# Kernel optimization log

Hardware: AMD Instinct MI355X
Metric: run time of the kernel (lower is better)

The kernel has to match this reference:

```python
import jax, jax.numpy as jnp
import numpy as np

B, N, D, H = 2, 2048, 1024, 16
HD = D // H

def setup_inputs() -> dict:
    key = jax.random.key(0)
    ks = jax.random.split(key, 8)
    s = lambda fan_in: 1.0 / np.sqrt(fan_in)
    return {
        "x": jax.random.normal(ks[0], (B, N, D), jnp.float32),
        "coverage": jax.random.uniform(ks[1], (B, N, 1), jnp.float32),
        "w_qkv": jax.random.normal(ks[2], (D, 3 * D), jnp.float32) * s(D),
        "w_out": jax.random.normal(ks[3], (D, D), jnp.float32) * s(D),
        "b_out": jnp.zeros((D,), jnp.float32),
        "w_ce1": jax.random.normal(ks[4], (1, D // 4), jnp.float32),
        "b_ce1": jnp.zeros((D // 4,), jnp.float32),
        "w_ce2": jax.random.normal(ks[5], (D // 4, H), jnp.float32) * s(D // 4),
        "b_ce2": jnp.zeros((H,), jnp.float32),
        "w_fg1": jax.random.normal(ks[6], (D, D // 4), jnp.float32) * s(D),
        "b_fg1": jnp.zeros((D // 4,), jnp.float32),
        "w_fg2": jax.random.normal(ks[7], (D // 4, 1), jnp.float32) * s(D // 4),
        "b_fg2": jnp.zeros((1,), jnp.float32),
    }

def reference(x, coverage, w_qkv, w_out, b_out, w_ce1, b_ce1, w_ce2, b_ce2,
              w_fg1, b_fg1, w_fg2, b_fg2):
    b, n, d = x.shape
    h = w_ce2.shape[1]
    hd = d // h
    scale = hd ** -0.5
    qkv = x @ w_qkv  # (B,N,3D)
    q, k, v = jnp.split(qkv, 3, axis=-1)
    q = q.reshape(b, n, h, hd).transpose(0, 2, 1, 3)  # (B,H,N,hd)
    k = k.reshape(b, n, h, hd).transpose(0, 2, 1, 3)
    v = v.reshape(b, n, h, hd).transpose(0, 2, 1, 3)
    attn = jnp.einsum("bhnd,bhmd->bhnm", q, k) * scale  # (B,H,N,N)
    # coverage bias: MLP(1 -> D/4 -> H), broadcast over query dim
    cov = jax.nn.silu(coverage @ w_ce1 + b_ce1) @ w_ce2 + b_ce2  # (B,N,H)
    cov_bias = cov.transpose(0, 2, 1)[:, :, None, :]  # (B,H,1,N)
    # fusion gate on mean-pooled features
    x_pooled = x.mean(axis=1)  # (B,D)
    g = jax.nn.sigmoid(jax.nn.silu(x_pooled @ w_fg1 + b_fg1) @ w_fg2 + b_fg2)  # (B,1)
    g = g[:, :, None, None]  # (B,1,1,1)
    # g*(attn+bias) + (1-g)*attn == attn + g*bias (exact same math)
    attn = attn + g * cov_bias
    attn = jax.nn.softmax(attn, axis=-1)
    out = jnp.einsum("bhnm,bhmd->bhnd", attn, v)  # (B,H,N,hd)
    out = out.transpose(0, 2, 1, 3).reshape(b, n, d)
    return out @ w_out + b_out
```

## Files before the change

### kernel.cpp

```cpp
#include <hip/hip_runtime.h>
#include <math.h>

typedef __bf16 bf16_t;
typedef __bf16 bf16x8 __attribute__((ext_vector_type(8)));
typedef __bf16 bf16x4 __attribute__((ext_vector_type(4)));
typedef float f32x4 __attribute__((ext_vector_type(4)));

#define MFMA16(a, b, c) __builtin_amdgcn_mfma_f32_16x16x32_bf16((a), (b), (c), 0, 0, 0)

constexpr int Bc = 2, Nc = 2048, Dc = 1024, Hc = 16, HDc = 64;
constexpr float C1 = 0.18033688011112042f;
constexpr float LOG2E = 1.4426950408889634f;

__device__ __forceinline__ void glds16(const bf16_t* g, bf16_t* l) {
    __builtin_amdgcn_global_load_lds(
        (const __attribute__((address_space(1))) unsigned int*)g,
        (__attribute__((address_space(3))) unsigned int*)l, 16, 0, 0);
}

__device__ __forceinline__ void tr64_body(const float* __restrict__ src,
                                          bf16_t* __restrict__ dst, int R, int C,
                                          int bx, int by, bf16_t* tile, int t) {
    int r0 = by * 64, c0 = bx * 64;
    int cl = t & 63, rl = t >> 6;
#pragma unroll
    for (int p = 0; p < 16; ++p) {
        int r = p * 4 + rl;
        tile[r * 66 + cl] = (bf16_t)src[(size_t)(r0 + r) * C + c0 + cl];
    }
    __syncthreads();
#pragma unroll
    for (int p = 0; p < 16; ++p) {
        int r = p * 4 + rl;
        dst[(size_t)(c0 + r) * R + r0 + cl] = tile[cl * 66 + r];
    }
}

__global__ __launch_bounds__(256) void prep(const float* __restrict__ x,
                                            bf16_t* __restrict__ Xb,
                                            const float* __restrict__ w_qkv,
                                            bf16_t* __restrict__ Wt,
                                            const float* __restrict__ w_out,
                                            bf16_t* __restrict__ WoT,
                                            float* __restrict__ pooled,
                                            const float* __restrict__ coverage,
                                            const float* __restrict__ w_ce1,
                                            const float* __restrict__ b_ce1,
                                            const float* __restrict__ w_ce2,
                                            const float* __restrict__ b_ce2,
                                            float* __restrict__ cbias) {
    __shared__ __align__(16) float smem[8768];
    int bid = blockIdx.x, t = threadIdx.x;

    if (bid < 64) {
        float* w1s = smem;
        float* b1s = smem + 256;
        float* w2s = smem + 512;
        float* part = smem + 4608;
        int b = bid >> 5, n0 = (bid & 31) * 64;
        w1s[t] = w_ce1[t];
        b1s[t] = b_ce1[t];
        {
            float4* w2v = (float4*)w2s;
            const float4* g4 = (const float4*)w_ce2;
#pragma unroll
            for (int i = 0; i < 4; ++i) w2v[i * 256 + t] = g4[i * 256 + t];
        }
        __syncthreads();
        int wv = t >> 6, lane2 = t & 63;
        float c = coverage[b * 2048 + n0 + lane2];
        float acc[16];
#pragma unroll
        for (int hh = 0; hh < 16; ++hh) acc[hh] = 0.f;
        for (int jj = 0; jj < 64; ++jj) {
            int j = wv * 64 + jj;
            float tv = fmaf(c, w1s[j], b1s[j]);
            tv = tv / (1.0f + __expf(-tv));
#pragma unroll
            for (int hh = 0; hh < 16; ++hh)
                acc[hh] = fmaf(tv, w2s[j * 16 + hh], acc[hh]);
        }
#pragma unroll
        for (int hh = 0; hh < 16; ++hh) part[lane2 * 65 + wv * 16 + hh] = acc[hh];
        __syncthreads();
#pragma unroll
        for (int i = 0; i < 4; ++i) {
            int idx = t + i * 256;
            int nl = idx >> 4, hh = idx & 15;
            const float* pr = part + nl * 65 + hh;
            float s = pr[0] + pr[16] + pr[32] + pr[48];
            cbias[((size_t)b * 16 + hh) * 2048 + n0 + nl] = LOG2E * (s + b_ce2[hh]);
        }
    } else if (bid < 320) {
        int blk = bid - 64;
        int b = blk >> 7, ch = blk & 127;
        int c = t * 4;
        float s0 = 0.f, s1 = 0.f, s2 = 0.f, s3 = 0.f;
        for (int rr = 0; rr < 16; ++rr) {
            float4 v = *(const float4*)(x + (size_t)(b * Nc + ch * 16 + rr) * Dc + c);
            s0 += v.x; s1 += v.y; s2 += v.z; s3 += v.w;
        }
        atomicAdd(&pooled[b * Dc + c + 0], s0);
        atomicAdd(&pooled[b * Dc + c + 1], s1);
        atomicAdd(&pooled[b * Dc + c + 2], s2);
        atomicAdd(&pooled[b * Dc + c + 3], s3);
    } else if (bid < 1088) {
        int bb = bid - 320;
        tr64_body(w_qkv, Wt, 1024, 3072, bb % 48, bb / 48, (bf16_t*)smem, t);
    } else if (bid < 1344) {
        int bb = bid - 1088;
        tr64_body(w_out, WoT, 1024, 1024, bb & 15, bb >> 4, (bf16_t*)smem, t);
    } else {
        int base = (bid - 1344) * 4096 + t * 4;
#pragma unroll
        for (int c = 0; c < 4; ++c) {
            int i = base + c * 1024;
            float4 v = *(const float4*)(x + i);
            bf16x4 o = { (bf16_t)v.x, (bf16_t)v.y, (bf16_t)v.z, (bf16_t)v.w };
            *(bf16x4*)(Xb + i) = o;
        }
    }
}

__global__ __launch_bounds__(256) void qkv_gemm(const bf16_t* __restrict__ Xb,
                                                const bf16_t* __restrict__ Wt,
                                                bf16_t* __restrict__ Q,
                                                bf16_t* __restrict__ Kb,
                                                bf16_t* __restrict__ Vt,
                                                const float* __restrict__ pooled,
                                                const float* __restrict__ w_fg1,
                                                const float* __restrict__ b_fg1,
                                                const float* __restrict__ w_fg2,
                                                float* __restrict__ hacc) {
    __shared__ __align__(16) bf16_t At[2][128 * 32];
    __shared__ __align__(16) bf16_t Bt[2][128 * 32];
    int t = threadIdx.x;

    if (blockIdx.y == 24) {
        __shared__ float red[4];
        int blk = blockIdx.x;
        int b = blk >> 4, jb = (blk & 15) * 16;
        for (int jj = 0; jj < 16; ++jj) {
            int j = jb + jj;
            float p = 0.f;
#pragma unroll
            for (int i = 0; i < 4; ++i) {
                int d = t * 4 + i;
                p += pooled[b * 1024 + d] * w_fg1[d * 256 + j];
            }
#pragma unroll
            for (int off = 32; off > 0; off >>= 1) p += __shfl_down(p, off);
            if ((t & 63) == 0) red[t >> 6] = p;
            __syncthreads();
            if (t == 0) {
                float hj = (red[0] + red[1] + red[2] + red[3]) * (1.0f / 2048.0f) + b_fg1[j];
                hj = hj / (1.0f + __expf(-hj));
                atomicAdd(&hacc[b], hj * w_fg2[j]);
            }
            __syncthreads();
        }
        return;
    }

    int w = t >> 6, lane = t & 63;
    int l16 = lane & 15, quad = lane >> 4;
    int wm = w & 1, wx = w >> 1;
    int m0 = blockIdx.x * 128;
    int n0 = blockIdx.y * 128;
    f32x4 acc[4][4] = {};
    int sw = (l16 >> 2) & 3;

    int arow[2], asc[2], aoff[2];
#pragma unroll
    for (int i = 0; i < 2; ++i) {
        int fb = i * 4096 + w * 1024;
        int f = fb + lane * 16;
        int row = f >> 6;
        int ch = (f >> 4) & 3;
        arow[i] = row;
        asc[i] = ch ^ ((row >> 2) & 3);
        aoff[i] = fb >> 1;
    }
    auto stage = [&](int k0, int bf) {
#pragma unroll
        for (int i = 0; i < 2; ++i) {
            glds16(Wt + (size_t)(n0 + arow[i]) * 1024 + k0 + asc[i] * 8, At[bf] + aoff[i]);
            glds16(Xb + (size_t)(m0 + arow[i]) * 1024 + k0 + asc[i] * 8, Bt[bf] + aoff[i]);
        }
    };

    stage(0, 0);
    for (int ks = 0; ks < 32; ++ks) {
        int sel = ks & 1;
        asm volatile("s_waitcnt lgkmcnt(0)" ::: "memory");
        __builtin_amdgcn_s_barrier();
        if (ks + 1 < 32) {
            stage((ks + 1) * 32, sel ^ 1);
            asm volatile("s_waitcnt vmcnt(4)" ::: "memory");
        } else {
            asm volatile("s_waitcnt vmcnt(0)" ::: "memory");
        }
        __builtin_amdgcn_s_barrier();
        __builtin_amdgcn_sched_barrier(0);

        const bf16_t* Ab = At[sel];
        const bf16_t* Bb = Bt[sel];
        bf16x8 afr[4], bfr[4];
#pragma unroll
        for (int mi = 0; mi < 4; ++mi)
            afr[mi] = *(const bf16x8*)(Ab + (wm * 64 + mi * 16 + l16) * 32 + ((quad ^ sw) * 8));
#pragma unroll
        for (int ni = 0; ni < 4; ++ni)
            bfr[ni] = *(const bf16x8*)(Bb + (wx * 64 + ni * 16 + l16) * 32 + ((quad ^ sw) * 8));
        __builtin_amdgcn_s_setprio(1);
#pragma unroll
        for (int mi = 0; mi < 4; ++mi)
#pragma unroll
            for (int ni = 0; ni < 4; ++ni)
                acc[mi][ni] = MFMA16(afr[mi], bfr[ni], acc[mi][ni]);
        __builtin_amdgcn_s_setprio(0);
    }

    int sec = n0 >> 10;
    float scq = (sec == 0) ? C1 : 1.0f;
#pragma unroll
    for (int mi = 0; mi < 4; ++mi) {
        int gc = n0 + wm * 64 + mi * 16 + quad * 4;
        int dcol = gc & 1023;
        int h = dcol >> 6, hd = dcol & 63;
#pragma unroll
        for (int ni = 0; ni < 4; ++ni) {
            int gx = m0 + wx * 64 + ni * 16 + l16;
            int b = gx >> 11, n = gx & 2047;
            size_t bh = (size_t)(b * 16 + h);
            if (sec == 2) {
#pragma unroll
                for (int r = 0; r < 4; ++r)
                    Vt[(bh * 64 + hd + r) * 2048 + n] = (bf16_t)acc[mi][ni][r];
            } else {
                bf16x4 pk = { (bf16_t)(acc[mi][ni][0] * scq), (bf16_t)(acc[mi][ni][1] * scq),
                              (bf16_t)(acc[mi][ni][2] * scq), (bf16_t)(acc[mi][ni][3] * scq) };
                bf16_t* dst = (sec == 0 ? Q : Kb);
                *(bf16x4*)(dst + (bh * 2048 + n) * 64 + hd) = pk;
            }
        }
    }
}

__global__ __launch_bounds__(256) void attn_k(const bf16_t* __restrict__ Q,
                                              const bf16_t* __restrict__ Kb,
                                              const bf16_t* __restrict__ Vt,
                                              const float* __restrict__ cbias,
                                              const float* __restrict__ hacc,
                                              const float* __restrict__ b_fg2,
                                              bf16_t* __restrict__ O) {
    __shared__ __align__(16) bf16_t kbuf[2][64 * 64];
    __shared__ __align__(16) bf16_t vbuf[2][64 * 64];
    __shared__ __align__(16) float ball[2048];
    int t = threadIdx.x, w = t >> 6, lane = t & 63;
    int l16 = lane & 15, quad = lane >> 4;
    int bh = blockIdx.y;
    int b = bh >> 4, h = bh & 15;
    int qa = blockIdx.x * 128 + w * 32;
    const bf16_t* Qh = Q + (size_t)bh * 2048 * 64;
    const bf16_t* Kh = Kb + (size_t)bh * 2048 * 64;
    const bf16_t* Vh = Vt + (size_t)bh * 64 * 2048;
    const float* bih = cbias + (size_t)bh * 2048;
    float g = 1.0f / (1.0f + __expf(-(hacc[b] + b_fg2[0])));

#pragma unroll
    for (int c = 0; c < 2; ++c) {
        float4 v = *(const float4*)(bih + c * 1024 + t * 4);
        float4 sv = { v.x * g, v.y * g, v.z * g, v.w * g };
        *(float4*)(ball + c * 1024 + t * 4) = sv;
    }

    int fb0 = w * 2048, fb1 = fb0 + 1024;
    int f0 = fb0 + lane * 16, f1 = fb1 + lane * 16;
    int krow0 = f0 >> 7, kch0 = ((f0 >> 4) & 7) ^ (krow0 & 7);
    int krow1 = f1 >> 7, kch1 = ((f1 >> 4) & 7) ^ (krow1 & 7);

    bf16x8 qf[2][2];
#pragma unroll
    for (int qt = 0; qt < 2; ++qt)
#pragma unroll
        for (int dh = 0; dh < 2; ++dh)
            qf[qt][dh] = *(const bf16x8*)(Qh + (size_t)(qa + qt * 16 + l16) * 64 + dh * 32 + quad * 8);

    f32x4 o[2][4] = {};
    f32x4 lacc[2] = {};
    bf16x8 onesb;
#pragma unroll
    for (int i = 0; i < 8; ++i) onesb[i] = (bf16_t)1.0f;
    int swl = l16 & 7;
    int qh = quad >> 1, ql = quad & 1;

    int bk0 = l16 * 64 + ((quad ^ swl) * 8);
    int bk1 = l16 * 64 + (((4 + quad) ^ swl) * 8);
    int bv0 = l16 * 64 + ql * 4 + ((qh ^ swl) * 8);
    int bv1 = l16 * 64 + ql * 4 + (((2 + qh) ^ swl) * 8);
    int bv2 = l16 * 64 + ql * 4 + (((4 + qh) ^ swl) * 8);
    int bv3 = l16 * 64 + ql * 4 + (((6 + qh) ^ swl) * 8);

    auto stage = [&](int tile_, int bf) {
        int jn = tile_ * 64;
        glds16(Kh + (size_t)(jn + krow0) * 64 + kch0 * 8, &kbuf[bf][fb0 >> 1]);
        glds16(Kh + (size_t)(jn + krow1) * 64 + kch1 * 8, &kbuf[bf][fb1 >> 1]);
        glds16(Vh + (size_t)krow0 * 2048 + jn + kch0 * 8, &vbuf[bf][fb0 >> 1]);
        glds16(Vh + (size_t)krow1 * 2048 + jn + kch1 * 8, &vbuf[bf][fb1 >> 1]);
    };

    stage(0, 0);

    for (int it = 0; it < 32; ++it) {
        int sel = it & 1, j0 = it * 64;
        asm volatile("s_waitcnt lgkmcnt(0)" ::: "memory");
        __builtin_amdgcn_s_barrier();
        if (it + 1 < 32) {
            stage(it + 1, sel ^ 1);
            asm volatile("s_waitcnt vmcnt(4)" ::: "memory");
        } else {
            asm volatile("s_waitcnt vmcnt(0)" ::: "memory");
        }
        __builtin_amdgcn_s_barrier();
        __builtin_amdgcn_sched_barrier(0);

        const bf16_t* kb = &kbuf[sel][0];
        const bf16_t* vb = &vbuf[sel][0];

        f32x4 s[2][4];
        __builtin_amdgcn_s_setprio(1);
#pragma unroll
        for (int kt = 0; kt < 4; ++kt) {
            f32x4 bi = *(const f32x4*)(ball + j0 + kt * 16 + quad * 4);
            bf16x8 kf0 = *(const bf16x8*)(kb + kt * 1024 + bk0);
            bf16x8 kf1 = *(const bf16x8*)(kb + kt * 1024 + bk1);
#pragma unroll
            for (int qt = 0; qt < 2; ++qt) {
                s[qt][kt] = MFMA16(kf0, qf[qt][0], bi);
                s[qt][kt] = MFMA16(kf1, qf[qt][1], s[qt][kt]);
            }
        }
        __builtin_amdgcn_s_setprio(0);

        bf16x8 pf[2][2];
#pragma unroll
        for (int qt = 0; qt < 2; ++qt) {
#pragma unroll
            for (int kt = 0; kt < 4; ++kt)
#pragma unroll
                for (int r = 0; r < 4; ++r)
                    s[qt][kt][r] = __builtin_amdgcn_exp2f(s[qt][kt][r]);
#pragma unroll
            for (int pv = 0; pv < 2; ++pv) {
                bf16x8 tmp;
#pragma unroll
                for (int i = 0; i < 4; ++i) {
                    tmp[i]     = (bf16_t)s[qt][2 * pv][i];
                    tmp[i + 4] = (bf16_t)s[qt][2 * pv + 1][i];
                }
                pf[qt][pv] = tmp;
            }
        }

        __builtin_amdgcn_s_setprio(1);
#pragma unroll
        for (int qt = 0; qt < 2; ++qt) {
            lacc[qt] = MFMA16(pf[qt][0], onesb, lacc[qt]);
            lacc[qt] = MFMA16(pf[qt][1], onesb, lacc[qt]);
        }
#pragma unroll
        for (int dt = 0; dt < 4; ++dt) {
            bf16x4 va0 = *(const bf16x4*)(vb + dt * 1024 + bv0);
            bf16x4 vc0 = *(const bf16x4*)(vb + dt * 1024 + bv1);
            bf16x8 vf0 = __builtin_shufflevector(va0, vc0, 0, 1, 2, 3, 4, 5, 6, 7);
            bf16x4 va1 = *(const bf16x4*)(vb + dt * 1024 + bv2);
            bf16x4 vc1 = *(const bf16x4*)(vb + dt * 1024 + bv3);
            bf16x8 vf1 = __builtin_shufflevector(va1, vc1, 0, 1, 2, 3, 4, 5, 6, 7);
#pragma unroll
            for (int qt = 0; qt < 2; ++qt) {
                o[qt][dt] = MFMA16(pf[qt][0], vf0, o[qt][dt]);
                o[qt][dt] = MFMA16(pf[qt][1], vf1, o[qt][dt]);
            }
        }
        __builtin_amdgcn_s_setprio(0);
    }

#pragma unroll
    for (int qt = 0; qt < 2; ++qt) {
        f32x4 rinv;
#pragma unroll
        for (int r = 0; r < 4; ++r) rinv[r] = 1.0f / lacc[qt][r];
#pragma unroll
        for (int dt = 0; dt < 4; ++dt)
#pragma unroll
            for (int r = 0; r < 4; ++r) {
                int row = qa + qt * 16 + quad * 4 + r;
                O[(size_t)(b * 2048 + row) * 1024 + h * 64 + dt * 16 + l16] =
                    (bf16_t)(o[qt][dt][r] * rinv[r]);
            }
    }
}

__global__ __launch_bounds__(256) void out_gemm(const bf16_t* __restrict__ A,
                                                const bf16_t* __restrict__ Wt,
                                                const float* __restrict__ bias,
                                                float* __restrict__ Cout) {
    __shared__ __align__(16) bf16_t At[2][128 * 32];
    __shared__ __align__(16) bf16_t Bt[2][128 * 32];
    int t = threadIdx.x, w = t >> 6, lane = t & 63;
    int l16 = lane & 15, quad = lane >> 4;
    int wm = w & 1, wx = w >> 1;
    int m0 = blockIdx.x * 128;
    int n0 = blockIdx.y * 128;
    f32x4 acc[4][4] = {};
    int sw = (l16 >> 2) & 3;

    int arow[2], asc[2], aoff[2];
#pragma unroll
    for (int i = 0; i < 2; ++i) {
        int fb = i * 4096 + w * 1024;
        int f = fb + lane * 16;
        int row = f >> 6;
        int ch = (f >> 4) & 3;
        arow[i] = row;
        asc[i] = ch ^ ((row >> 2) & 3);
        aoff[i] = fb >> 1;
    }
    auto stage = [&](int k0, int bf) {
#pragma unroll
        for (int i = 0; i < 2; ++i) {
            glds16(Wt + (size_t)(n0 + arow[i]) * 1024 + k0 + asc[i] * 8, At[bf] + aoff[i]);
            glds16(A + (size_t)(m0 + arow[i]) * 1024 + k0 + asc[i] * 8, Bt[bf] + aoff[i]);
        }
    };

    stage(0, 0);
    for (int ks = 0; ks < 32; ++ks) {
        int sel = ks & 1;
        asm volatile("s_waitcnt lgkmcnt(0)" ::: "memory");
        __builtin_amdgcn_s_barrier();
        if (ks + 1 < 32) {
            stage((ks + 1) * 32, sel ^ 1);
            asm volatile("s_waitcnt vmcnt(4)" ::: "memory");
        } else {
            asm volatile("s_waitcnt vmcnt(0)" ::: "memory");
        }
        __builtin_amdgcn_s_barrier();
        __builtin_amdgcn_sched_barrier(0);

        const bf16_t* Ab = At[sel];
        const bf16_t* Bb = Bt[sel];
        bf16x8 afr[4], bfr[4];
#pragma unroll
        for (int mi = 0; mi < 4; ++mi)
            afr[mi] = *(const bf16x8*)(Ab + (wm * 64 + mi * 16 + l16) * 32 + ((quad ^ sw) * 8));
#pragma unroll
        for (int ni = 0; ni < 4; ++ni)
            bfr[ni] = *(const bf16x8*)(Bb + (wx * 64 + ni * 16 + l16) * 32 + ((quad ^ sw) * 8));
        __builtin_amdgcn_s_setprio(1);
#pragma unroll
        for (int mi = 0; mi < 4; ++mi)
#pragma unroll
            for (int ni = 0; ni < 4; ++ni)
                acc[mi][ni] = MFMA16(afr[mi], bfr[ni], acc[mi][ni]);
        __builtin_amdgcn_s_setprio(0);
    }

#pragma unroll
    for (int mi = 0; mi < 4; ++mi) {
        int gc = n0 + wm * 64 + mi * 16 + quad * 4;
        float4 bv = *(const float4*)(bias + gc);
#pragma unroll
        for (int ni = 0; ni < 4; ++ni) {
            int gx = m0 + wx * 64 + ni * 16 + l16;
            float4 ov = { acc[mi][ni][0] + bv.x, acc[mi][ni][1] + bv.y,
                          acc[mi][ni][2] + bv.z, acc[mi][ni][3] + bv.w };
            *(float4*)(Cout + (size_t)gx * 1024 + gc) = ov;
        }
    }
}

extern "C" void kernel_launch(void* const* d_in, const int* in_sizes, int n_in,
                              void* d_out, int out_size, void* d_ws, size_t ws_size,
                              hipStream_t stream) {
    const float* x     = (const float*)d_in[0];
    const float* cov   = (const float*)d_in[1];
    const float* w_qkv = (const float*)d_in[2];
    const float* w_out = (const float*)d_in[3];
    const float* b_out = (const float*)d_in[4];
    const float* w_ce1 = (const float*)d_in[5];
    const float* b_ce1 = (const float*)d_in[6];
    const float* w_ce2 = (const float*)d_in[7];
    const float* b_ce2 = (const float*)d_in[8];
    const float* w_fg1 = (const float*)d_in[9];
    const float* b_fg1 = (const float*)d_in[10];
    const float* w_fg2 = (const float*)d_in[11];
    const float* b_fg2 = (const float*)d_in[12];

    char* ws = (char*)d_ws;
    bf16_t* Wt     = (bf16_t*)(ws);
    bf16_t* WoT    = (bf16_t*)(ws + 6291456);
    bf16_t* Xb     = (bf16_t*)(ws + 8388608);
    bf16_t* Qb     = (bf16_t*)(ws + 16777216);
    bf16_t* Kbb    = (bf16_t*)(ws + 25165824);
    bf16_t* Vt     = (bf16_t*)(ws + 33554432);
    bf16_t* Ob     = (bf16_t*)(ws + 41943040);
    float*  pooled = (float*)(ws + 50331648);
    float*  hacc   = (float*)(ws + 50339840);
    float*  biasb  = (float*)(ws + 50340096);

    hipMemsetAsync(pooled, 0, 8200, stream);
    prep<<<2368, 256, 0, stream>>>(x, Xb, w_qkv, Wt, w_out, WoT, pooled,
                                   cov, w_ce1, b_ce1, w_ce2, b_ce2, biasb);
    qkv_gemm<<<dim3(32, 25), 256, 0, stream>>>(Xb, Wt, Qb, Kbb, Vt,
                                               pooled, w_fg1, b_fg1, w_fg2, hacc);
    attn_k<<<dim3(16, 32), 256, 0, stream>>>(Qb, Kbb, Vt, biasb, hacc, b_fg2, Ob);
    out_gemm<<<dim3(32, 8), 256, 0, stream>>>(Ob, WoT, b_out, (float*)d_out);
}
```

Before: 246.0 us.

## Triple-buffer LDS staging in GEMMs and attention; fuse pooling with bf16 cast

All three main kernels (QKV GEMM, attention, output GEMM) move from double-buffered to triple-buffered LDS staging. Each now prefetches two tiles ahead and drops one barrier per iteration, so global-to-LDS loads overlap compute more deeply. The prep kernel also merges the mean-pool reduction with the x-to-bf16 cast, so x is read once instead of twice, and the grid shrinks accordingly. The cost is more LDS per block, which may reduce occupancy, and the vmcnt(4) wait now has two stages in flight, so correctness depends on how many loads each stage issues.

```diff
diff --git a/kernel.cpp b/kernel.cpp
--- a/kernel.cpp
+++ b/kernel.cpp
@@ -91,34 +91,29 @@
             float s = pr[0] + pr[16] + pr[32] + pr[48];
             cbias[((size_t)b * 16 + hh) * 2048 + n0 + nl] = LOG2E * (s + b_ce2[hh]);
         }
-    } else if (bid < 320) {
-        int blk = bid - 64;
-        int b = blk >> 7, ch = blk & 127;
-        int c = t * 4;
+    } else if (bid < 832) {
+        int bb = bid - 64;
+        tr64_body(w_qkv, Wt, 1024, 3072, bb % 48, bb / 48, (bf16_t*)smem, t);
+    } else if (bid < 1088) {
+        int bb = bid - 832;
+        tr64_body(w_out, WoT, 1024, 1024, bb & 15, bb >> 4, (bf16_t*)smem, t);
+    } else {
+        int blk = bid - 1088;
+        int b = blk >> 7;
+        int rbase = blk * 16;
+        int d = t * 4;
         float s0 = 0.f, s1 = 0.f, s2 = 0.f, s3 = 0.f;
         for (int rr = 0; rr < 16; ++rr) {
-            float4 v = *(const float4*)(x + (size_t)(b * Nc + ch * 16 + rr) * Dc + c);
+            size_t off = (size_t)(rbase + rr) * 1024 + d;
+            float4 v = *(const float4*)(x + off);
             s0 += v.x; s1 += v.y; s2 += v.z; s3 += v.w;
-        }
-        atomicAdd(&pooled[b * Dc + c + 0], s0);
-        atomicAdd(&pooled[b * Dc + c + 1], s1);
-        atomicAdd(&pooled[b * Dc + c + 2], s2);
-        atomicAdd(&pooled[b * Dc + c + 3], s3);
-    } else if (bid < 1088) {
-        int bb = bid - 320;
-        tr64_body(w_qkv, Wt, 1024, 3072, bb % 48, bb / 48, (bf16_t*)smem, t);
-    } else if (bid < 1344) {
-        int bb = bid - 1088;
-        tr64_body(w_out, WoT, 1024, 1024, bb & 15, bb >> 4, (bf16_t*)smem, t);
-    } else {
-        int base = (bid - 1344) * 4096 + t * 4;
-#pragma unroll
-        for (int c = 0; c < 4; ++c) {
-            int i = base + c * 1024;
-            float4 v = *(const float4*)(x + i);
             bf16x4 o = { (bf16_t)v.x, (bf16_t)v.y, (bf16_t)v.z, (bf16_t)v.w };
-            *(bf16x4*)(Xb + i) = o;
-        }
+            *(bf16x4*)(Xb + off) = o;
+        }
+        atomicAdd(&pooled[b * 1024 + d + 0], s0);
+        atomicAdd(&pooled[b * 1024 + d + 1], s1);
+        atomicAdd(&pooled[b * 1024 + d + 2], s2);
+        atomicAdd(&pooled[b * 1024 + d + 3], s3);
     }
 }
 
@@ -132,8 +127,8 @@
                                                 const float* __restrict__ b_fg1,
                                                 const float* __restrict__ w_fg2,
                                                 float* __restrict__ hacc) {
-    __shared__ __align__(16) bf16_t At[2][128 * 32];
-    __shared__ __align__(16) bf16_t Bt[2][128 * 32];
+    __shared__ __align__(16) bf16_t At[3][128 * 32];
+    __shared__ __align__(16) bf16_t Bt[3][128 * 32];
     int t = threadIdx.x;
 
     if (blockIdx.y == 24) {
@@ -190,21 +185,20 @@
     };
 
     stage(0, 0);
+    stage(32, 1);
+    int cur = 0, nxt = 2;
     for (int ks = 0; ks < 32; ++ks) {
-        int sel = ks & 1;
-        asm volatile("s_waitcnt lgkmcnt(0)" ::: "memory");
-        __builtin_amdgcn_s_barrier();
         if (ks + 1 < 32) {
-            stage((ks + 1) * 32, sel ^ 1);
             asm volatile("s_waitcnt vmcnt(4)" ::: "memory");
         } else {
             asm volatile("s_waitcnt vmcnt(0)" ::: "memory");
         }
         __builtin_amdgcn_s_barrier();
+        if (ks + 2 < 32) stage((ks + 2) * 32, nxt);
         __builtin_amdgcn_sched_barrier(0);
 
-        const bf16_t* Ab = At[sel];
-        const bf16_t* Bb = Bt[sel];
+        const bf16_t* Ab = At[cur];
+        const bf16_t* Bb = Bt[cur];
         bf16x8 afr[4], bfr[4];
 #pragma unroll
         for (int mi = 0; mi < 4; ++mi)
@@ -219,6 +213,8 @@
             for (int ni = 0; ni < 4; ++ni)
                 acc[mi][ni] = MFMA16(afr[mi], bfr[ni], acc[mi][ni]);
         __builtin_amdgcn_s_setprio(0);
+        cur = (cur == 2) ? 0 : cur + 1;
+        nxt = (nxt == 2) ? 0 : nxt + 1;
     }
 
     int sec = n0 >> 10;
@@ -254,8 +250,8 @@
                                               const float* __restrict__ hacc,
                                               const float* __restrict__ b_fg2,
                                               bf16_t* __restrict__ O) {
-    __shared__ __align__(16) bf16_t kbuf[2][64 * 64];
-    __shared__ __align__(16) bf16_t vbuf[2][64 * 64];
+    __shared__ __align__(16) bf16_t kbuf[3][64 * 64];
+    __shared__ __align__(16) bf16_t vbuf[3][64 * 64];
     __shared__ __align__(16) float ball[2048];
     int t = threadIdx.x, w = t >> 6, lane = t & 63;
     int l16 = lane & 15, quad = lane >> 4;
@@ -311,22 +307,23 @@
     };
 
     stage(0, 0);
+    stage(1, 1);
+    asm volatile("s_waitcnt lgkmcnt(0)" ::: "memory");
+    int cur = 0, nxt = 2;
 
     for (int it = 0; it < 32; ++it) {
-        int sel = it & 1, j0 = it * 64;
-        asm volatile("s_waitcnt lgkmcnt(0)" ::: "memory");
-        __builtin_amdgcn_s_barrier();
+        int j0 = it * 64;
         if (it + 1 < 32) {
-            stage(it + 1, sel ^ 1);
             asm volatile("s_waitcnt vmcnt(4)" ::: "memory");
         } else {
             asm volatile("s_waitcnt vmcnt(0)" ::: "memory");
         }
         __builtin_amdgcn_s_barrier();
+        if (it + 2 < 32) stage(it + 2, nxt);
         __builtin_amdgcn_sched_barrier(0);
 
-        const bf16_t* kb = &kbuf[sel][0];
-        const bf16_t* vb = &vbuf[sel][0];
+        const bf16_t* kb = &kbuf[cur][0];
+        const bf16_t* vb = &vbuf[cur][0];
 
         f32x4 s[2][4];
         __builtin_amdgcn_s_setprio(1);
@@ -384,6 +381,8 @@
             }
         }
         __builtin_amdgcn_s_setprio(0);
+        cur = (cur == 2) ? 0 : cur + 1;
+        nxt = (nxt == 2) ? 0 : nxt + 1;
     }
 
 #pragma unroll
@@ -406,8 +405,8 @@
                                                 const bf16_t* __restrict__ Wt,
                                                 const float* __restrict__ bias,
                                                 float* __restrict__ Cout) {
-    __shared__ __align__(16) bf16_t At[2][128 * 32];
-    __shared__ __align__(16) bf16_t Bt[2][128 * 32];
+    __shared__ __align__(16) bf16_t At[3][128 * 32];
+    __shared__ __align__(16) bf16_t Bt[3][128 * 32];
     int t = threadIdx.x, w = t >> 6, lane = t & 63;
     int l16 = lane & 15, quad = lane >> 4;
     int wm = w & 1, wx = w >> 1;
@@ -436,21 +435,20 @@
     };
 
     stage(0, 0);
+    stage(32, 1);
+    int cur = 0, nxt = 2;
     for (int ks = 0; ks < 32; ++ks) {
-        int sel = ks & 1;
-        asm volatile("s_waitcnt lgkmcnt(0)" ::: "memory");
-        __builtin_amdgcn_s_barrier();
         if (ks + 1 < 32) {
-            stage((ks + 1) * 32, sel ^ 1);
             asm volatile("s_waitcnt vmcnt(4)" ::: "memory");
         } else {
             asm volatile("s_waitcnt vmcnt(0)" ::: "memory");
         }
         __builtin_amdgcn_s_barrier();
+        if (ks + 2 < 32) stage((ks + 2) * 32, nxt);
         __builtin_amdgcn_sched_barrier(0);
 
-        const bf16_t* Ab = At[sel];
-        const bf16_t* Bb = Bt[sel];
+        const bf16_t* Ab = At[cur];
+        const bf16_t* Bb = Bt[cur];
         bf16x8 afr[4], bfr[4];
 #pragma unroll
         for (int mi = 0; mi < 4; ++mi)
@@ -465,6 +463,8 @@
             for (int ni = 0; ni < 4; ++ni)
                 acc[mi][ni] = MFMA16(afr[mi], bfr[ni], acc[mi][ni]);
         __builtin_amdgcn_s_setprio(0);
+        cur = (cur == 2) ? 0 : cur + 1;
+        nxt = (nxt == 2) ? 0 : nxt + 1;
     }
 
 #pragma unroll
@@ -511,7 +511,7 @@
     float*  biasb  = (float*)(ws + 50340096);
 
     hipMemsetAsync(pooled, 0, 8200, stream);
-    prep<<<2368, 256, 0, stream>>>(x, Xb, w_qkv, Wt, w_out, WoT, pooled,
+    prep<<<1344, 256, 0, stream>>>(x, Xb, w_qkv, Wt, w_out, WoT, pooled,
                                    cov, w_ce1, b_ce1, w_ce2, b_ce2, biasb);
     qkv_gemm<<<dim3(32, 25), 256, 0, stream>>>(Xb, Wt, Qb, Kbb, Vt,
                                                pooled, w_fg1, b_fg1, w_fg2, hacc);
```

Measured after the change: 246.3 us. Within noise of the previous version (+0.1%).
